# Kernel tuning notes

Measured on AMD Instinct MI355X. Metric: run time of the kernel, lower is better.

The kernel has to match this reference:

```python
import jax, jax.numpy as jnp
import numpy as np

D_MODEL = 512
NHEAD = 8
WINDOW = 64


def setup_inputs() -> dict:
    key = jax.random.key(0)
    ks = jax.random.split(key, 5)
    d = D_MODEL
    x = jax.random.normal(ks[0], (8, 2048, d), dtype=jnp.float32)
    # nn.MultiheadAttention params: packed in-proj [3d, d] + bias [3d], out-proj [d, d] + bias [d]
    scale = 1.0 / np.sqrt(d)
    in_proj_w = jax.random.normal(ks[1], (3 * d, d), dtype=jnp.float32) * scale
    in_proj_b = jnp.zeros((3 * d,), dtype=jnp.float32)
    out_proj_w = jax.random.normal(ks[2], (d, d), dtype=jnp.float32) * scale
    out_proj_b = jnp.zeros((d,), dtype=jnp.float32)
    return {"x": x, "in_proj_w": in_proj_w, "in_proj_b": in_proj_b,
            "out_proj_w": out_proj_w, "out_proj_b": out_proj_b}


def reference(x, in_proj_w, in_proj_b, out_proj_w, out_proj_b):
    B, L, d = x.shape
    H = NHEAD
    dh = d // H
    # packed qkv projection (torch Linear: x @ W.T + b)
    qkv = jnp.einsum('bld,ed->ble', x, in_proj_w) + in_proj_b  # [B, L, 3d]
    q, k, v = jnp.split(qkv, 3, axis=-1)
    # split heads -> [B, H, L, dh]
    def heads(t):
        return t.reshape(B, L, H, dh).transpose(0, 2, 1, 3)
    q, k, v = heads(q), heads(k), heads(v)
    scores = jnp.einsum('bhqd,bhkd->bhqk', q, k) / jnp.sqrt(jnp.float32(dh))
    # banded mask: positions with |i-j| > window are masked out
    idx = jnp.arange(L)
    band = jnp.abs(idx[None, :] - idx[:, None]) > WINDOW  # [L, L] bool
    scores = jnp.where(band[None, None, :, :], jnp.float32(-jnp.inf), scores)
    p = jax.nn.softmax(scores, axis=-1)
    out = jnp.einsum('bhqk,bhkd->bhqd', p, v)  # [B, H, L, dh]
    out = out.transpose(0, 2, 1, 3).reshape(B, L, d)
    return jnp.einsum('bld,ed->ble', out, out_proj_w) + out_proj_b
```

## Files before the change

### kernel.cpp

```cpp
#include <hip/hip_runtime.h>

typedef __bf16 bf16x8 __attribute__((ext_vector_type(8)));
typedef unsigned short u16;
typedef unsigned short u16x8 __attribute__((ext_vector_type(8)));
typedef float f32x4 __attribute__((ext_vector_type(4)));

#define L_SEQ 2048
#define NQT   (L_SEQ / 128)

__device__ __forceinline__ float bf2f(u16 x) {
    unsigned u = ((unsigned)x) << 16;
    return __builtin_bit_cast(float, u);
}
__device__ __forceinline__ u16 f2bf(float f) {
    unsigned u = __builtin_bit_cast(unsigned, f);
    u += 0x7FFFu + ((u >> 16) & 1u);
    return (u16)(u >> 16);
}

__device__ __forceinline__ void gload_lds16(const u16* g, u16* l) {
    __builtin_amdgcn_global_load_lds(
        (const __attribute__((address_space(1))) void*)g,
        (__attribute__((address_space(3))) void*)l, 16, 0, 0);
}

__global__ void cvt_all(const float* __restrict__ x, const float* __restrict__ wi,
                        const float* __restrict__ wo, u16* __restrict__ xo,
                        u16* __restrict__ wio, u16* __restrict__ woo,
                        int nx8, int nwi8, int nwo8) {
    int i = blockIdx.x * blockDim.x + threadIdx.x;
    const float* src; u16* dst;
    if (i < nx8) { src = x; dst = xo; }
    else if (i < nx8 + nwi8) { i -= nx8; src = wi; dst = wio; }
    else if (i < nx8 + nwi8 + nwo8) { i -= nx8 + nwi8; src = wo; dst = woo; }
    else return;
    const float4* p = reinterpret_cast<const float4*>(src) + (size_t)i * 2;
    const float4 a = p[0], b = p[1];
    u16x8 r;
    r[0] = f2bf(a.x); r[1] = f2bf(a.y); r[2] = f2bf(a.z); r[3] = f2bf(a.w);
    r[4] = f2bf(b.x); r[5] = f2bf(b.y); r[6] = f2bf(b.z); r[7] = f2bf(b.w);
    *(reinterpret_cast<u16x8*>(dst) + i) = r;
}

template <bool OUT_BF16>
__launch_bounds__(256, 3)
__global__ void gemm_ring(const u16* __restrict__ A, const u16* __restrict__ W,
                          const float* __restrict__ bias, void* __restrict__ Cv,
                          int M, int N, int K) {
    __shared__ u16 As[3][128 * 32];
    __shared__ u16 Bs[3][128 * 32];

    const int tid   = threadIdx.x;
    const int lane  = tid & 63;
    const int wid   = tid >> 6;
    const int wm    = wid >> 1;
    const int wn    = wid & 1;
    const int row_l = lane & 15;
    const int grp   = lane >> 4;

    const int nwg  = gridDim.x * gridDim.y;
    const int hw   = blockIdx.y * gridDim.x + blockIdx.x;
    const int tile = (hw & 7) * (nwg >> 3) + (hw >> 3);
    const int m0 = (tile / gridDim.x) * 128;
    const int n0 = (tile % gridDim.x) * 128;

    const int srow = tid >> 2;
    const int scol = ((tid & 3) ^ ((tid >> 3) & 3)) * 8;
    const u16* gA = A + (size_t)(m0 + srow) * K + scol;
    const u16* gB = W + (size_t)(n0 + srow) * K + scol;

    f32x4 acc[4][4];
#pragma unroll
    for (int mi = 0; mi < 4; ++mi)
#pragma unroll
        for (int ni = 0; ni < 4; ++ni)
            acc[mi][ni] = (f32x4){0.f, 0.f, 0.f, 0.f};

    auto stage = [&](int buf, int kt) {
#pragma unroll
        for (int i = 0; i < 2; ++i) {
            gload_lds16(gA + (size_t)(i * 64) * K + kt * 32, &As[buf][i * 2048 + wid * 512]);
            gload_lds16(gB + (size_t)(i * 64) * K + kt * 32, &Bs[buf][i * 2048 + wid * 512]);
        }
    };

    const int rchunk = (grp ^ ((row_l >> 1) & 3)) * 8;

    auto compute = [&](int buf) {
        bf16x8 a[4], b[4];
#pragma unroll
        for (int mi = 0; mi < 4; ++mi)
            a[mi] = *reinterpret_cast<const bf16x8*>(
                &As[buf][(wm * 64 + mi * 16 + row_l) * 32 + rchunk]);
#pragma unroll
        for (int ni = 0; ni < 4; ++ni)
            b[ni] = *reinterpret_cast<const bf16x8*>(
                &Bs[buf][(wn * 64 + ni * 16 + row_l) * 32 + rchunk]);
        __builtin_amdgcn_s_setprio(1);
#pragma unroll
        for (int mi = 0; mi < 4; ++mi)
#pragma unroll
            for (int ni = 0; ni < 4; ++ni)
                acc[mi][ni] = __builtin_amdgcn_mfma_f32_16x16x32_bf16(a[mi], b[ni], acc[mi][ni], 0, 0, 0);
        __builtin_amdgcn_s_setprio(0);
    };

    const int NT = K >> 5;
    stage(0, 0);
    stage(1, 1);
    int cur = 0;
    for (int t = 0; t < NT; ++t) {
        if (t == NT - 1) asm volatile("s_waitcnt vmcnt(0)" ::: "memory");
        else             asm volatile("s_waitcnt vmcnt(4)" ::: "memory");
        __builtin_amdgcn_s_barrier();
        if (t + 2 < NT) {
            int st = cur + 2; if (st >= 3) st -= 3;
            stage(st, t + 2);
        }
        compute(cur);
        cur = cur + 1; if (cur >= 3) cur = 0;
    }

#pragma unroll
    for (int ni = 0; ni < 4; ++ni) {
        const int col = n0 + wn * 64 + ni * 16 + row_l;
        const float bsf = bias[col];
#pragma unroll
        for (int mi = 0; mi < 4; ++mi) {
#pragma unroll
            for (int r = 0; r < 4; ++r) {
                const int rowm = m0 + wm * 64 + mi * 16 + grp * 4 + r;
                const float v = acc[mi][ni][r] + bsf;
                if (OUT_BF16)
                    ((u16*)Cv)[(size_t)rowm * N + col] = f2bf(v);
                else
                    ((float*)Cv)[(size_t)rowm * N + col] = v;
            }
        }
    }
}

__launch_bounds__(512, 4)
__global__ void local_attn(const u16* __restrict__ qkv, u16* __restrict__ att) {
    __shared__ __align__(16) u16 Ks[256 * 64];
    __shared__ __align__(16) u16 Vt[64 * 256];
    __shared__ __align__(16) u16 Pl[8][512];

    const int tid   = threadIdx.x;
    const int lane  = tid & 63;
    const int wv    = tid >> 6;
    const int row_l = lane & 15;
    const int grp   = lane >> 4;
    const int qt = blockIdx.x, h = blockIdx.y, b = blockIdx.z;
    const int q0b = qt * 128;
    const int kstart = q0b - 64;
    const size_t base = (size_t)b * L_SEQ * 1536;
    const bool edge = (qt == 0) || (qt == NQT - 1);

    {
        const int r0 = tid >> 3;
        const int c  = tid & 7;
#pragma unroll
        for (int i = 0; i < 4; ++i) {
            const int row  = i * 64 + r0;
            const int keyg = min(max(kstart + row, 0), L_SEQ - 1);
            const int cg   = c ^ (row & 7);
            gload_lds16(qkv + base + (size_t)keyg * 1536 + 512 + h * 64 + cg * 8,
                        &Ks[i * 4096 + wv * 512]);
        }
    }
    {
#pragma unroll
        for (int i = 0; i < 4; ++i) {
            const int idx  = i * 512 + tid;
            const int row  = idx >> 3;
            const int c8   = idx & 7;
            const int keyg = min(max(kstart + row, 0), L_SEQ - 1);
            const u16x8 vu = *reinterpret_cast<const u16x8*>(
                qkv + base + (size_t)keyg * 1536 + 1024 + h * 64 + c8 * 8);
#pragma unroll
            for (int e = 0; e < 8; ++e) {
                const int d = c8 * 8 + e;
                Vt[d * 256 + (((row >> 3) ^ (d & 7)) * 8) + (row & 7)] = vu[e];
            }
        }
    }

    const int qrow_g = q0b + wv * 16 + row_l;
    const u16* qp = qkv + base + (size_t)qrow_g * 1536 + h * 64;
    const bf16x8 qf0 = *reinterpret_cast<const bf16x8*>(qp + grp * 8);
    const bf16x8 qf1 = *reinterpret_cast<const bf16x8*>(qp + 32 + grp * 8);

    __syncthreads();

    float m_r = -1e30f, l_r = 0.f;
    f32x4 acc[4];
#pragma unroll
    for (int ds = 0; ds < 4; ++ds) acc[ds] = (f32x4){0.f, 0.f, 0.f, 0.f};
    u16* Pw = Pl[wv];

    auto do_chunk = [&](int c, bool bandLo, bool bandHi, bool half, bool rng) {
        const int kcL = wv * 16 + 32 * c;
        const int kcG = kstart + kcL;
        const int nf = half ? 1 : 2;

        f32x4 s[2];
#pragma unroll
        for (int f = 0; f < 2; ++f) {
            if (f >= nf) break;
            const int rr = kcL + 16 * f + row_l;
            const bf16x8 ka = *reinterpret_cast<const bf16x8*>(
                &Ks[rr * 64 + ((grp ^ (rr & 7)) * 8)]);
            const bf16x8 kb = *reinterpret_cast<const bf16x8*>(
                &Ks[rr * 64 + (((grp + 4) ^ (rr & 7)) * 8)]);
            f32x4 z = (f32x4){0.f, 0.f, 0.f, 0.f};
            z = __builtin_amdgcn_mfma_f32_16x16x32_bf16(ka, qf0, z, 0, 0, 0);
            z = __builtin_amdgcn_mfma_f32_16x16x32_bf16(kb, qf1, z, 0, 0, 0);
            s[f] = z;
        }

        float p[2][4];
        float cmax = -1e30f;
#pragma unroll
        for (int f = 0; f < 2; ++f) {
            if (f >= nf) break;
#pragma unroll
            for (int r = 0; r < 4; ++r) {
                const int k = 16 * f + grp * 4 + r;
                bool ok = true;
                if (bandLo) ok = ok && (k >= row_l);
                if (bandHi) ok = ok && (k <= row_l);
                if (rng) { const int kg = kcG + k; ok = ok && (kg >= 0) && (kg < L_SEQ); }
                const float sv = ok ? s[f][r] * 0.125f : -1e30f;
                p[f][r] = sv;
                cmax = fmaxf(cmax, sv);
            }
        }
        cmax = fmaxf(cmax, __shfl_xor(cmax, 16, 64));
        cmax = fmaxf(cmax, __shfl_xor(cmax, 32, 64));
        const float mn  = fmaxf(m_r, cmax);
        const float scl = __expf(m_r - mn);
        m_r = mn;
        float lsum = 0.f;
#pragma unroll
        for (int f = 0; f < 2; ++f) {
            if (f >= nf) break;
#pragma unroll
            for (int r = 0; r < 4; ++r) {
                const float pv = (p[f][r] <= -1e29f) ? 0.f : __expf(p[f][r] - mn);
                p[f][r] = pv;
                lsum += pv;
            }
        }
        lsum += __shfl_xor(lsum, 16, 64);
        lsum += __shfl_xor(lsum, 32, 64);
        l_r = l_r * scl + lsum;

        float scl4[4];
#pragma unroll
        for (int r = 0; r < 4; ++r) scl4[r] = __shfl(scl, grp * 4 + r, 64);
#pragma unroll
        for (int ds = 0; ds < 4; ++ds)
#pragma unroll
            for (int r = 0; r < 4; ++r) acc[ds][r] *= scl4[r];

#pragma unroll
        for (int f = 0; f < 2; ++f)
#pragma unroll
            for (int r = 0; r < 4; ++r) {
                const int k = 16 * f + grp * 4 + r;
                const int slot = (k >> 3) ^ ((row_l >> 1) & 3);
                const float pv = (f < nf) ? p[f][r] : 0.f;
                Pw[row_l * 32 + slot * 8 + (k & 7)] = f2bf(pv);
            }
        const bf16x8 pa = *reinterpret_cast<const bf16x8*>(
            &Pw[row_l * 32 + ((grp ^ ((row_l >> 1) & 3)) * 8)]);

        int k0 = kcL + grp * 8;
        if (half) k0 = min(k0, 248);
#pragma unroll
        for (int ds = 0; ds < 4; ++ds) {
            const int d = ds * 16 + row_l;
            const bf16x8 vf = *reinterpret_cast<const bf16x8*>(
                &Vt[d * 256 + (((k0 >> 3) ^ (d & 7)) * 8)]);
            acc[ds] = __builtin_amdgcn_mfma_f32_16x16x32_bf16(pa, vf, acc[ds], 0, 0, 0);
        }
    };

    if (!edge) {
        do_chunk(0, true,  false, false, false);
        do_chunk(1, false, false, false, false);
        do_chunk(2, false, false, false, false);
        do_chunk(3, false, false, false, false);
        do_chunk(4, false, true,  true,  false);
    } else {
        const int kw = kstart + wv * 16;
        if (kw       > -32 && kw       < L_SEQ) do_chunk(0, true,  false, false, true);
        if (kw + 32  > -32 && kw + 32  < L_SEQ) do_chunk(1, false, false, false, true);
        if (kw + 64  > -32 && kw + 64  < L_SEQ) do_chunk(2, false, false, false, true);
        if (kw + 96  > -32 && kw + 96  < L_SEQ) do_chunk(3, false, false, false, true);
        if (kw + 128 > -32 && kw + 128 < L_SEQ) do_chunk(4, false, true,  true,  true);
    }

    const float inv = 1.f / l_r;
    float inv4[4];
#pragma unroll
    for (int r = 0; r < 4; ++r) inv4[r] = __shfl(inv, grp * 4 + r, 64);
    const int qg = q0b + wv * 16 + grp * 4;
#pragma unroll
    for (int r = 0; r < 4; ++r)
#pragma unroll
        for (int ds = 0; ds < 4; ++ds)
            att[(size_t)(b * L_SEQ + qg + r) * 512 + h * 64 + ds * 16 + row_l] =
                f2bf(acc[ds][r] * inv4[r]);
}

extern "C" void kernel_launch(void* const* d_in, const int* in_sizes, int n_in,
                              void* d_out, int out_size, void* d_ws, size_t ws_size,
                              hipStream_t stream) {
    const float* x     = (const float*)d_in[0];
    const float* w_in  = (const float*)d_in[1];
    const float* b_in  = (const float*)d_in[2];
    const float* w_out = (const float*)d_in[3];
    const float* b_out = (const float*)d_in[4];
    float* out = (float*)d_out;

    const int B = 8, L = L_SEQ;
    const int M = B * L;

    u16* qkv   = (u16*)d_ws;
    u16* att   = qkv   + (size_t)M * 1536;
    u16* x_bf  = att   + (size_t)M * 512;
    u16* wi_bf = x_bf  + (size_t)M * 512;
    u16* wo_bf = wi_bf + (size_t)1536 * 512;

    const int nx8  = M * 512 / 8;
    const int nwi8 = 1536 * 512 / 8;
    const int nwo8 = 512 * 512 / 8;
    const int ncvt = nx8 + nwi8 + nwo8;
    cvt_all<<<(ncvt + 255) / 256, 256, 0, stream>>>(x, w_in, w_out, x_bf, wi_bf, wo_bf,
                                                    nx8, nwi8, nwo8);

    gemm_ring<true><<<dim3(1536 / 128, M / 128), dim3(256), 0, stream>>>(
        x_bf, wi_bf, b_in, qkv, M, 1536, 512);

    local_attn<<<dim3(NQT, 8, B), dim3(512), 0, stream>>>(qkv, att);

    gemm_ring<false><<<dim3(512 / 128, M / 128), dim3(256), 0, stream>>>(
        att, wo_bf, b_out, out, M, 512, 512);
}
```

Measured before the change: 90.77 us.

## Enlarge GEMM tiles to 256x128 with 512 threads, add lazy softmax rescale

The GEMM kernel now uses 512-thread blocks computing 256x128 tiles, and its pipeline is reordered so fragments load from LDS before the next stage is issued, with separate waits and barriers. This cuts the number of workgroups and lets each B tile be reused across more rows. In attention, the online softmax skips the max update and accumulator rescale when no row's new max exceeds the running max by more than 8, saving exp and shuffle work. The V transpose swizzle adds a second XOR term to reduce LDS bank conflicts. Risks include lower occupancy and fewer blocks per device for the small out-projection, and slightly different numerics from the lazy rescale.

```diff
diff --git a/kernel.cpp b/kernel.cpp
--- a/kernel.cpp
+++ b/kernel.cpp
@@ -43,11 +43,11 @@
 }
 
 template <bool OUT_BF16>
-__launch_bounds__(256, 3)
-__global__ void gemm_ring(const u16* __restrict__ A, const u16* __restrict__ W,
-                          const float* __restrict__ bias, void* __restrict__ Cv,
-                          int M, int N, int K) {
-    __shared__ u16 As[3][128 * 32];
+__launch_bounds__(512, 4)
+__global__ void gemm_big(const u16* __restrict__ A, const u16* __restrict__ W,
+                         const float* __restrict__ bias, void* __restrict__ Cv,
+                         int M, int N, int K) {
+    __shared__ u16 As[3][256 * 32];
     __shared__ u16 Bs[3][128 * 32];
 
     const int tid   = threadIdx.x;
@@ -61,7 +61,7 @@
     const int nwg  = gridDim.x * gridDim.y;
     const int hw   = blockIdx.y * gridDim.x + blockIdx.x;
     const int tile = (hw & 7) * (nwg >> 3) + (hw >> 3);
-    const int m0 = (tile / gridDim.x) * 128;
+    const int m0 = (tile / gridDim.x) * 256;
     const int n0 = (tile % gridDim.x) * 128;
 
     const int srow = tid >> 2;
@@ -77,16 +77,21 @@
             acc[mi][ni] = (f32x4){0.f, 0.f, 0.f, 0.f};
 
     auto stage = [&](int buf, int kt) {
-#pragma unroll
-        for (int i = 0; i < 2; ++i) {
-            gload_lds16(gA + (size_t)(i * 64) * K + kt * 32, &As[buf][i * 2048 + wid * 512]);
-            gload_lds16(gB + (size_t)(i * 64) * K + kt * 32, &Bs[buf][i * 2048 + wid * 512]);
-        }
+        gload_lds16(gA + (size_t)kt * 32,                   &As[buf][0]    + wid * 512);
+        gload_lds16(gA + (size_t)128 * K + (size_t)kt * 32, &As[buf][4096] + wid * 512);
+        gload_lds16(gB + (size_t)kt * 32,                   &Bs[buf][0]    + wid * 512);
     };
 
     const int rchunk = (grp ^ ((row_l >> 1) & 3)) * 8;
 
-    auto compute = [&](int buf) {
+    const int NT = K >> 5;
+    stage(0, 0);
+    stage(1, 1);
+    asm volatile("s_waitcnt vmcnt(3)" ::: "memory");
+    __builtin_amdgcn_s_barrier();
+
+    int buf = 0;
+    for (int kt = 0; kt < NT; ++kt) {
         bf16x8 a[4], b[4];
 #pragma unroll
         for (int mi = 0; mi < 4; ++mi)
@@ -96,6 +101,16 @@
         for (int ni = 0; ni < 4; ++ni)
             b[ni] = *reinterpret_cast<const bf16x8*>(
                 &Bs[buf][(wn * 64 + ni * 16 + row_l) * 32 + rchunk]);
+
+        if (kt + 2 < NT) {
+            int st = buf + 2; if (st >= 3) st -= 3;
+            stage(st, kt + 2);
+        }
+        if (kt < NT - 2)       asm volatile("s_waitcnt vmcnt(3)" ::: "memory");
+        else if (kt == NT - 2) asm volatile("s_waitcnt vmcnt(0)" ::: "memory");
+        __builtin_amdgcn_s_barrier();
+        asm volatile("s_waitcnt lgkmcnt(0)" ::: "memory");
+        __builtin_amdgcn_sched_barrier(0);
         __builtin_amdgcn_s_setprio(1);
 #pragma unroll
         for (int mi = 0; mi < 4; ++mi)
@@ -103,22 +118,8 @@
             for (int ni = 0; ni < 4; ++ni)
                 acc[mi][ni] = __builtin_amdgcn_mfma_f32_16x16x32_bf16(a[mi], b[ni], acc[mi][ni], 0, 0, 0);
         __builtin_amdgcn_s_setprio(0);
-    };
-
-    const int NT = K >> 5;
-    stage(0, 0);
-    stage(1, 1);
-    int cur = 0;
-    for (int t = 0; t < NT; ++t) {
-        if (t == NT - 1) asm volatile("s_waitcnt vmcnt(0)" ::: "memory");
-        else             asm volatile("s_waitcnt vmcnt(4)" ::: "memory");
         __builtin_amdgcn_s_barrier();
-        if (t + 2 < NT) {
-            int st = cur + 2; if (st >= 3) st -= 3;
-            stage(st, t + 2);
-        }
-        compute(cur);
-        cur = cur + 1; if (cur >= 3) cur = 0;
+        buf = buf + 1; if (buf >= 3) buf = 0;
     }
 
 #pragma unroll
@@ -181,7 +182,8 @@
 #pragma unroll
             for (int e = 0; e < 8; ++e) {
                 const int d = c8 * 8 + e;
-                Vt[d * 256 + (((row >> 3) ^ (d & 7)) * 8) + (row & 7)] = vu[e];
+                const int slot = (row >> 3) ^ (d & 7) ^ ((d >> 3) & 7);
+                Vt[d * 256 + slot * 8 + (row & 7)] = vu[e];
             }
         }
     }
@@ -238,16 +240,26 @@
         }
         cmax = fmaxf(cmax, __shfl_xor(cmax, 16, 64));
         cmax = fmaxf(cmax, __shfl_xor(cmax, 32, 64));
-        const float mn  = fmaxf(m_r, cmax);
-        const float scl = __expf(m_r - mn);
-        m_r = mn;
+
+        const bool need = !__all(cmax <= m_r + 8.f);
+        float mu;
+        float scl = 1.f;
+        if (need) {
+            const float mn = fmaxf(m_r, cmax);
+            scl = __expf(m_r - mn);
+            m_r = mn;
+            mu  = mn;
+        } else {
+            mu = m_r;
+        }
+
         float lsum = 0.f;
 #pragma unroll
         for (int f = 0; f < 2; ++f) {
             if (f >= nf) break;
 #pragma unroll
             for (int r = 0; r < 4; ++r) {
-                const float pv = (p[f][r] <= -1e29f) ? 0.f : __expf(p[f][r] - mn);
+                const float pv = (p[f][r] <= -1e29f) ? 0.f : __expf(p[f][r] - mu);
                 p[f][r] = pv;
                 lsum += pv;
             }
@@ -256,13 +268,15 @@
         lsum += __shfl_xor(lsum, 32, 64);
         l_r = l_r * scl + lsum;
 
-        float scl4[4];
-#pragma unroll
-        for (int r = 0; r < 4; ++r) scl4[r] = __shfl(scl, grp * 4 + r, 64);
-#pragma unroll
-        for (int ds = 0; ds < 4; ++ds)
-#pragma unroll
-            for (int r = 0; r < 4; ++r) acc[ds][r] *= scl4[r];
+        if (need) {
+            float scl4[4];
+#pragma unroll
+            for (int r = 0; r < 4; ++r) scl4[r] = __shfl(scl, grp * 4 + r, 64);
+#pragma unroll
+            for (int ds = 0; ds < 4; ++ds)
+#pragma unroll
+                for (int r = 0; r < 4; ++r) acc[ds][r] *= scl4[r];
+        }
 
 #pragma unroll
         for (int f = 0; f < 2; ++f)
@@ -281,8 +295,9 @@
 #pragma unroll
         for (int ds = 0; ds < 4; ++ds) {
             const int d = ds * 16 + row_l;
+            const int slot = (k0 >> 3) ^ (d & 7) ^ ((d >> 3) & 7);
             const bf16x8 vf = *reinterpret_cast<const bf16x8*>(
-                &Vt[d * 256 + (((k0 >> 3) ^ (d & 7)) * 8)]);
+                &Vt[d * 256 + slot * 8]);
             acc[ds] = __builtin_amdgcn_mfma_f32_16x16x32_bf16(pa, vf, acc[ds], 0, 0, 0);
         }
     };
@@ -341,11 +356,11 @@
     cvt_all<<<(ncvt + 255) / 256, 256, 0, stream>>>(x, w_in, w_out, x_bf, wi_bf, wo_bf,
                                                     nx8, nwi8, nwo8);
 
-    gemm_ring<true><<<dim3(1536 / 128, M / 128), dim3(256), 0, stream>>>(
+    gemm_big<true><<<dim3(1536 / 128, M / 256), dim3(512), 0, stream>>>(
         x_bf, wi_bf, b_in, qkv, M, 1536, 512);
 
     local_attn<<<dim3(NQT, 8, B), dim3(512), 0, stream>>>(qkv, att);
 
-    gemm_ring<false><<<dim3(512 / 128, M / 128), dim3(256), 0, stream>>>(
+    gemm_big<false><<<dim3(512 / 128, M / 256), dim3(512), 0, stream>>>(
         att, wo_bf, b_out, out, M, 512, 512);
 }
```

After: 87.76 us. -3.3%, faster.
